# Kernel tuning notes

Hardware: AMD Instinct MI355X
Metric: run time of the kernel (lower is better)

## Reference

```python
import jax, jax.numpy as jnp
import numpy as np

B, IN, H = 16384, 1024, 1024


def setup_inputs() -> dict:
    key = jax.random.key(0)
    ks = jax.random.split(key, 7)
    s_in = 1.0 / np.sqrt(IN)
    s_h = 1.0 / np.sqrt(H)
    return {
        "x": jax.random.normal(ks[0], (B, IN), jnp.float32),
        "h0": jax.random.normal(ks[1], (B, H), jnp.float32),
        "c0": jax.random.normal(ks[2], (B, H), jnp.float32),
        # gate order along leading dim: f, i, o, g
        "wi": jax.random.uniform(ks[3], (4, H, IN), jnp.float32, -s_in, s_in),
        "bi": jax.random.uniform(ks[4], (4, H), jnp.float32, -s_in, s_in),
        "wh": jax.random.uniform(ks[5], (4, H, H), jnp.float32, -s_h, s_h),
        "bh": jax.random.uniform(ks[6], (4, H), jnp.float32, -s_h, s_h),
    }


def reference(x, h0, c0, wi, bi, wh, bh):
    # pre-activations for all 4 gates in two fused GEMMs: [b, 4, h]
    z = (jnp.einsum("bi,ghi->bgh", x, wi) + bi
         + jnp.einsum("bj,ghj->bgh", h0, wh) + bh)
    f = jax.nn.sigmoid(z[:, 0])   # forget gate
    i = jax.nn.sigmoid(z[:, 1])   # input gate
    o = jax.nn.sigmoid(z[:, 2])   # output gate
    g = jnp.tanh(z[:, 3])         # candidates
    ct = f * c0 + i * g
    ht = o * jnp.tanh(ct)
    return ht, ct
```

## Files before the change

kernel.cpp:

```cpp
#include <hip/hip_runtime.h>
#include <hip/hip_bf16.h>
#include <stdint.h>

#define B_ROWS 16384
#define K_DIM  2048
#define H_DIM  1024
#define N_DIM  4096
#define KB     (K_DIM * 2)
#define NT     (K_DIM / 64)
#define BUFSZ  65536u

using f32x4  = __attribute__((ext_vector_type(4))) float;
using bf16x8 = __attribute__((ext_vector_type(8))) __bf16;

__device__ __forceinline__ unsigned short f2bf(float f) {
    union { float f; unsigned u; } v; v.f = f;
    unsigned r = v.u + 0x7fffu + ((v.u >> 16) & 1u);
    return (unsigned short)(r >> 16);
}

__device__ __forceinline__ void gload16(const void* g, const void* l) {
    __builtin_amdgcn_global_load_lds(
        (const __attribute__((address_space(1))) void*)g,
        (__attribute__((address_space(3))) void*)l,
        16, 0, 0);
}

__device__ __forceinline__ float rcp1p(float e) {
    return __builtin_amdgcn_rcpf(1.f + e);
}

__global__ void pack_a_kernel(const float* __restrict__ x, const float* __restrict__ h0,
                              unsigned short* __restrict__ A) {
    int tid = blockIdx.x * 256 + threadIdx.x;
    int64_t idx = (int64_t)tid * 4;
    int b = (int)(idx >> 11);
    int k = (int)(idx & 2047);
    const float* src = (k < 1024) ? (x + (int64_t)b * 1024 + k)
                                  : (h0 + (int64_t)b * 1024 + (k - 1024));
    float4 v = *(const float4*)src;
    ushort4 o;
    o.x = f2bf(v.x); o.y = f2bf(v.y); o.z = f2bf(v.z); o.w = f2bf(v.w);
    *(ushort4*)(A + idx) = o;
}

__global__ void pack_w_kernel(const float* __restrict__ wi, const float* __restrict__ wh,
                              const float* __restrict__ bi, const float* __restrict__ bh,
                              unsigned short* __restrict__ W, float* __restrict__ bias) {
    int tid = blockIdx.x * 256 + threadIdx.x;
    int64_t idx = (int64_t)tid * 4;
    int r = (int)(idx >> 11);
    int k = (int)(idx & 2047);
    int h = r >> 2, g = r & 3;
    const float* src = (k < 1024)
        ? (wi + (int64_t)g * 1048576 + (int64_t)h * 1024 + k)
        : (wh + (int64_t)g * 1048576 + (int64_t)h * 1024 + (k - 1024));
    float4 v = *(const float4*)src;
    ushort4 o;
    o.x = f2bf(v.x); o.y = f2bf(v.y); o.z = f2bf(v.z); o.w = f2bf(v.w);
    *(ushort4*)(W + idx) = o;
    if (k == 0) bias[r] = bi[g * 1024 + h] + bh[g * 1024 + h];
}


#define SCHED0  __builtin_amdgcn_sched_barrier(0)
#define FENCE   asm volatile("" ::: "memory")
#define BAR     __builtin_amdgcn_s_barrier()

#define PH_PRE  do { FENCE; BAR; \
                     asm volatile("s_waitcnt lgkmcnt(0)" ::: "memory"); \
                     SCHED0; __builtin_amdgcn_s_setprio(1); } while (0)
#define PH_POST do { __builtin_amdgcn_s_setprio(0); SCHED0; FENCE; BAR; } while (0)
#define PH_POST_V do { __builtin_amdgcn_s_setprio(0); SCHED0; \
                       asm volatile("s_waitcnt vmcnt(4)" ::: "memory"); \
                       SCHED0; FENCE; BAR; } while (0)

__global__ __launch_bounds__(512, 2) void lstm_gemm_fused(
    const unsigned short* __restrict__ A, const unsigned short* __restrict__ W,
    const float* __restrict__ bias, const float* __restrict__ c0,
    float* __restrict__ ht, float* __restrict__ ct)
{
    __shared__ char sm[131072];

    const int tid = threadIdx.x;
    const int l   = tid & 63;
    const int w   = tid >> 6;
    const int wm  = w >> 2;
    const int wn  = w & 3;

    const int bid = blockIdx.x;
    const int nid = (bid & 7) * 128 + (bid >> 3);
    const int bm  = nid >> 4;
    const int bn  = nid & 15;

    f32x4 acc[8][4];
#pragma unroll
    for (int i = 0; i < 8; ++i)
#pragma unroll
        for (int j = 0; j < 4; ++j) acc[i][j] = (f32x4){0.f, 0.f, 0.f, 0.f};

    const int srow = w * 16 + (l >> 2);
    const int scb  = ((l & 3) << 4) ^ (l & 32);
    const char* Asrc = (const char*)A + (size_t)(bm * 256 + srow) * KB + scb;
    const char* Wsrc = (const char*)W + (size_t)(bn * 256 + srow) * KB + scb;
    const uint32_t wL = (uint32_t)w * 1024u;

#define STAGE_A(KK, BOFF) do { \
    gload16(Asrc + (KK) * 64,            sm + (BOFF) + (KK) * 16384u + wL); \
    gload16(Asrc + (KK) * 64 + 128 * KB, sm + (BOFF) + (KK) * 16384u + 8192u + wL); \
} while (0)
#define STAGE_B(KK, BOFF) do { \
    gload16(Wsrc + (KK) * 64,            sm + (BOFF) + 32768u + (KK) * 16384u + wL); \
    gload16(Wsrc + (KK) * 64 + 128 * KB, sm + (BOFF) + 32768u + (KK) * 16384u + 8192u + wL); \
} while (0)

    const int rr = l & 15, kg = l >> 4;
    const uint32_t loff = (uint32_t)rr * 64u + (((uint32_t)kg * 16u) ^ (uint32_t)((rr & 8) << 2));
    const uint32_t Ard = (uint32_t)wm * 8192u + loff;
    const uint32_t Brd = 32768u + (uint32_t)wn * 4096u + loff;

    bf16x8 aL[4], aH[4], bb0[4], bb1[4];

#define RD_A4(BOFF, KK, MB, ARR) do { \
    _Pragma("unroll") \
    for (int i_ = 0; i_ < 4; ++i_) \
        ARR[i_] = *(const bf16x8*)(sm + (BOFF) + (KK) * 16384u + Ard + ((MB) + i_) * 1024u); \
} while (0)
#define RD_B4(BOFF, KK, BRR) do { \
    _Pragma("unroll") \
    for (int i_ = 0; i_ < 4; ++i_) \
        BRR[i_] = *(const bf16x8*)(sm + (BOFF) + (KK) * 16384u + Brd + i_ * 1024u); \
} while (0)

#define MFMA16H(ARR, MB, BRR) do { \
    _Pragma("unroll") \
    for (int mf_ = 0; mf_ < 4; ++mf_) \
        _Pragma("unroll") \
        for (int nf_ = 0; nf_ < 4; ++nf_) \
            acc[(MB) + mf_][nf_] = __builtin_amdgcn_mfma_f32_16x16x32_bf16( \
                ARR[mf_], BRR[nf_], acc[(MB) + mf_][nf_], 0, 0, 0); \
} while (0)

    STAGE_A(0, 0u); STAGE_B(0, 0u);
    STAGE_A(1, 0u); STAGE_B(1, 0u);
    Asrc += 128; Wsrc += 128;
    asm volatile("s_waitcnt vmcnt(4)" ::: "memory");
    SCHED0; FENCE; BAR;

#define DO_TILE(CUR, NXT) do { \
     \
    RD_A4(CUR, 0, 0, aL); RD_B4(CUR, 0, bb0); \
    STAGE_A(0, NXT); \
    PH_PRE; MFMA16H(aL, 0, bb0); PH_POST; \
     \
    RD_A4(CUR, 0, 4, aH); \
    STAGE_B(0, NXT); \
    PH_PRE; MFMA16H(aH, 4, bb0); PH_POST_V; \
     \
    RD_A4(CUR, 1, 0, aL); RD_B4(CUR, 1, bb1); \
    STAGE_A(1, NXT); \
    PH_PRE; MFMA16H(aL, 0, bb1); PH_POST; \
     \
    RD_A4(CUR, 1, 4, aH); \
    STAGE_B(1, NXT); \
    PH_PRE; MFMA16H(aH, 4, bb1); PH_POST_V; \
    Asrc += 128; Wsrc += 128; \
} while (0)

#pragma unroll 1
    for (int tt = 0; tt < NT; tt += 2) {
        DO_TILE(0u, BUFSZ);
        DO_TILE(BUFSZ, 0u);
    }

    asm volatile("s_waitcnt vmcnt(0) lgkmcnt(0)" ::: "memory");
    FENCE; BAR;

    float* ep = (float*)(void*)sm + w * 1088;
    const int hbase = bn * 64 + wn * 16;
    const int rbase = bm * 256 + wm * 128;

#pragma unroll
    for (int mf = 0; mf < 8; ++mf) {
#pragma unroll
        for (int nf = 0; nf < 4; ++nf)
#pragma unroll
            for (int r = 0; r < 4; ++r)
                ep[((l >> 4) * 4 + r) * 68 + nf * 16 + (l & 15)] = acc[mf][nf][r];

#pragma unroll
        for (int it = 0; it < 4; ++it) {
            const int row = (l >> 4) + it * 4;
            const int hs  = l & 15;
            f32x4 z = *(const f32x4*)(ep + row * 68 + hs * 4);
            const int hg = hbase + hs;
            const float4 bz = ((const float4*)bias)[hg];
            const int brow = rbase + mf * 16 + row;

            float zf = z.x + bz.x;
            float zi = z.y + bz.y;
            float zo = z.z + bz.z;
            float zg = z.w + bz.w;

            float fg = rcp1p(__expf(-zf));
            float ig = rcp1p(__expf(-zi));
            float og = rcp1p(__expf(-zo));
            float gg = 2.f * rcp1p(__expf(-2.f * zg)) - 1.f;

            int64_t oi = (int64_t)brow * H_DIM + hg;
            float c  = fg * c0[oi] + ig * gg;
            float hh = og * (2.f * rcp1p(__expf(-2.f * c)) - 1.f);
            ct[oi] = c;
            ht[oi] = hh;
        }
    }
}

extern "C" void kernel_launch(void* const* d_in, const int* in_sizes, int n_in,
                              void* d_out, int out_size, void* d_ws, size_t ws_size,
                              hipStream_t stream) {
    const float* x  = (const float*)d_in[0];
    const float* h0 = (const float*)d_in[1];
    const float* c0 = (const float*)d_in[2];
    const float* wi = (const float*)d_in[3];
    const float* bi = (const float*)d_in[4];
    const float* wh = (const float*)d_in[5];
    const float* bh = (const float*)d_in[6];

    float* ht = (float*)d_out;
    float* ct = ht + (int64_t)B_ROWS * H_DIM;

    char* ws = (char*)d_ws;
    unsigned short* A  = (unsigned short*)ws;
    unsigned short* Wp = (unsigned short*)(ws + (64u << 20));
    float*          bs = (float*)(ws + (80u << 20));

    pack_a_kernel<<<32768, 256, 0, stream>>>(x, h0, A);
    pack_w_kernel<<<8192, 256, 0, stream>>>(wi, wh, bi, bh, Wp, bs);

    lstm_gemm_fused<<<1024, 512, 0, stream>>>(A, Wp, bs, c0, ht, ct);
}
```

Before: 313.9 us.

## Load weight fragments directly into registers instead of staging through LDS

```diff
diff --git a/kernel.cpp b/kernel.cpp
--- a/kernel.cpp
+++ b/kernel.cpp
@@ -8,7 +8,8 @@
 #define N_DIM  4096
 #define KB     (K_DIM * 2)
 #define NT     (K_DIM / 64)
-#define BUFSZ  65536u
+#define BUF0   0u
+#define BUF1   32768u
 
 using f32x4  = __attribute__((ext_vector_type(4))) float;
 using bf16x8 = __attribute__((ext_vector_type(8))) __bf16;
@@ -63,16 +64,15 @@
 }
 
 
-#define SCHED0  __builtin_amdgcn_sched_barrier(0)
 #define FENCE   asm volatile("" ::: "memory")
 #define BAR     __builtin_amdgcn_s_barrier()
+#define SCHED0  __builtin_amdgcn_sched_barrier(0)
 
 #define PH_PRE  do { FENCE; BAR; \
                      asm volatile("s_waitcnt lgkmcnt(0)" ::: "memory"); \
                      SCHED0; __builtin_amdgcn_s_setprio(1); } while (0)
-#define PH_POST do { __builtin_amdgcn_s_setprio(0); SCHED0; FENCE; BAR; } while (0)
 #define PH_POST_V do { __builtin_amdgcn_s_setprio(0); SCHED0; \
-                       asm volatile("s_waitcnt vmcnt(4)" ::: "memory"); \
+                       asm volatile("s_waitcnt vmcnt(6)" ::: "memory"); \
                        SCHED0; FENCE; BAR; } while (0)
 
 __global__ __launch_bounds__(512, 2) void lstm_gemm_fused(
@@ -80,7 +80,7 @@
     const float* __restrict__ bias, const float* __restrict__ c0,
     float* __restrict__ ht, float* __restrict__ ct)
 {
-    __shared__ char sm[131072];
+    __shared__ char sm[65536];
 
     const int tid = threadIdx.x;
     const int l   = tid & 63;
@@ -90,8 +90,8 @@
 
     const int bid = blockIdx.x;
     const int nid = (bid & 7) * 128 + (bid >> 3);
-    const int bm  = nid >> 4;
-    const int bn  = nid & 15;
+    const int bm  = nid & 63;
+    const int bn  = nid >> 6;
 
     f32x4 acc[8][4];
 #pragma unroll
@@ -102,75 +102,70 @@
     const int srow = w * 16 + (l >> 2);
     const int scb  = ((l & 3) << 4) ^ (l & 32);
     const char* Asrc = (const char*)A + (size_t)(bm * 256 + srow) * KB + scb;
-    const char* Wsrc = (const char*)W + (size_t)(bn * 256 + srow) * KB + scb;
     const uint32_t wL = (uint32_t)w * 1024u;
 
 #define STAGE_A(KK, BOFF) do { \
     gload16(Asrc + (KK) * 64,            sm + (BOFF) + (KK) * 16384u + wL); \
     gload16(Asrc + (KK) * 64 + 128 * KB, sm + (BOFF) + (KK) * 16384u + 8192u + wL); \
 } while (0)
-#define STAGE_B(KK, BOFF) do { \
-    gload16(Wsrc + (KK) * 64,            sm + (BOFF) + 32768u + (KK) * 16384u + wL); \
-    gload16(Wsrc + (KK) * 64 + 128 * KB, sm + (BOFF) + 32768u + (KK) * 16384u + 8192u + wL); \
-} while (0)
+
+    const char* Bsrc = (const char*)W
+        + (size_t)(bn * 256 + wn * 64 + (l & 15)) * KB + (l >> 4) * 16;
+
+#define LOADB(KK, BANK) do { \
+    _Pragma("unroll") \
+    for (int nf_ = 0; nf_ < 4; ++nf_) \
+        BANK[nf_] = *(const bf16x8*)(Bsrc + (size_t)nf_ * (16 * KB) + (KK) * 64); \
+} while (0)
+#define BUMP do { Asrc += 128; Bsrc += 128; } while (0)
 
     const int rr = l & 15, kg = l >> 4;
     const uint32_t loff = (uint32_t)rr * 64u + (((uint32_t)kg * 16u) ^ (uint32_t)((rr & 8) << 2));
     const uint32_t Ard = (uint32_t)wm * 8192u + loff;
-    const uint32_t Brd = 32768u + (uint32_t)wn * 4096u + loff;
-
-    bf16x8 aL[4], aH[4], bb0[4], bb1[4];
-
-#define RD_A4(BOFF, KK, MB, ARR) do { \
+
+    bf16x8 af[8], bbAe[4], bbBe[4], bbAo[4], bbBo[4];
+
+#define RD_A8(BOFF, KK) do { \
     _Pragma("unroll") \
-    for (int i_ = 0; i_ < 4; ++i_) \
-        ARR[i_] = *(const bf16x8*)(sm + (BOFF) + (KK) * 16384u + Ard + ((MB) + i_) * 1024u); \
-} while (0)
-#define RD_B4(BOFF, KK, BRR) do { \
+    for (int i_ = 0; i_ < 8; ++i_) \
+        af[i_] = *(const bf16x8*)(sm + (BOFF) + (KK) * 16384u + Ard + i_ * 1024u); \
+} while (0)
+
+#define MFMA32(BANK) do { \
     _Pragma("unroll") \
-    for (int i_ = 0; i_ < 4; ++i_) \
-        BRR[i_] = *(const bf16x8*)(sm + (BOFF) + (KK) * 16384u + Brd + i_ * 1024u); \
-} while (0)
-
-#define MFMA16H(ARR, MB, BRR) do { \
-    _Pragma("unroll") \
-    for (int mf_ = 0; mf_ < 4; ++mf_) \
+    for (int mf_ = 0; mf_ < 8; ++mf_) \
         _Pragma("unroll") \
         for (int nf_ = 0; nf_ < 4; ++nf_) \
-            acc[(MB) + mf_][nf_] = __builtin_amdgcn_mfma_f32_16x16x32_bf16( \
-                ARR[mf_], BRR[nf_], acc[(MB) + mf_][nf_], 0, 0, 0); \
-} while (0)
-
-    STAGE_A(0, 0u); STAGE_B(0, 0u);
-    STAGE_A(1, 0u); STAGE_B(1, 0u);
-    Asrc += 128; Wsrc += 128;
+            acc[mf_][nf_] = __builtin_amdgcn_mfma_f32_16x16x32_bf16( \
+                af[mf_], BANK[nf_], acc[mf_][nf_], 0, 0, 0); \
+} while (0)
+
+    STAGE_A(0, BUF0);
+    STAGE_A(1, BUF0);
+    LOADB(0, bbAe);
+    LOADB(1, bbBe);
+    BUMP;
     asm volatile("s_waitcnt vmcnt(4)" ::: "memory");
     SCHED0; FENCE; BAR;
 
-#define DO_TILE(CUR, NXT) do { \
+#define DO_TILE(CUR, NXT, BA_C, BB_C, BA_N, BB_N) do { \
      \
-    RD_A4(CUR, 0, 0, aL); RD_B4(CUR, 0, bb0); \
+    RD_A8(CUR, 0); \
     STAGE_A(0, NXT); \
-    PH_PRE; MFMA16H(aL, 0, bb0); PH_POST; \
+    LOADB(0, BA_N); \
+    PH_PRE; MFMA32(BA_C); PH_POST_V; \
      \
-    RD_A4(CUR, 0, 4, aH); \
-    STAGE_B(0, NXT); \
-    PH_PRE; MFMA16H(aH, 4, bb0); PH_POST_V; \
-     \
-    RD_A4(CUR, 1, 0, aL); RD_B4(CUR, 1, bb1); \
+    RD_A8(CUR, 1); \
     STAGE_A(1, NXT); \
-    PH_PRE; MFMA16H(aL, 0, bb1); PH_POST; \
-     \
-    RD_A4(CUR, 1, 4, aH); \
-    STAGE_B(1, NXT); \
-    PH_PRE; MFMA16H(aH, 4, bb1); PH_POST_V; \
-    Asrc += 128; Wsrc += 128; \
+    LOADB(1, BB_N); \
+    PH_PRE; MFMA32(BB_C); PH_POST_V; \
+    BUMP; \
 } while (0)
 
 #pragma unroll 1
     for (int tt = 0; tt < NT; tt += 2) {
-        DO_TILE(0u, BUFSZ);
-        DO_TILE(BUFSZ, 0u);
+        DO_TILE(BUF0, BUF1, bbAe, bbBe, bbAo, bbBo);
+        DO_TILE(BUF1, BUF0, bbAo, bbBo, bbAe, bbBe);
     }
 
     asm volatile("s_waitcnt vmcnt(0) lgkmcnt(0)" ::: "memory");
```

New measurement: 444.3 us. 1.42x slower.
